# Kernel tuning notes

Measured on AMD Instinct MI355X. Metric: run time of the kernel, lower is better.

## Reference

```python
import jax, jax.numpy as jnp
import numpy as np
import math

N = 8192        # n_cells
D_IN = 512      # input_dim
D_H = 1024      # hidden_dim
N_F = 8         # min(8, N//2)
FS = N // N_F   # faction size
SYNC = 0.15
DEBATE = 0.15
TWO_PI = 2.0 * math.pi


def setup_inputs() -> dict:
    key = jax.random.key(0)
    ks = jax.random.split(key, 10)
    phases = jax.random.uniform(ks[0], (N,), dtype=jnp.float32) * TWO_PI
    omegas = jax.random.normal(ks[1], (N,), dtype=jnp.float32) * 0.5 + 1.0
    coupling = jax.random.normal(ks[2], (N, N), dtype=jnp.float32) * 0.01
    K = jnp.asarray(2.0, dtype=jnp.float32)
    # Linear weights stored as [in, out]
    w_p2h = jax.random.normal(ks[3], (2, D_H), dtype=jnp.float32) * (1.0 / math.sqrt(2.0))
    b_p2h = jnp.zeros((D_H,), dtype=jnp.float32)
    w_enc1 = jax.random.normal(ks[4], (D_H + D_IN, D_H), dtype=jnp.float32) * (1.0 / math.sqrt(D_H + D_IN))
    b_enc1 = jnp.zeros((D_H,), dtype=jnp.float32)
    w_enc2 = jax.random.normal(ks[5], (D_H, D_H), dtype=jnp.float32) * (1.0 / math.sqrt(D_H))
    b_enc2 = jnp.zeros((D_H,), dtype=jnp.float32)
    w_out = jax.random.normal(ks[6], (D_H, D_IN), dtype=jnp.float32) * (1.0 / math.sqrt(D_H))
    b_out = jnp.zeros((D_IN,), dtype=jnp.float32)
    x = jax.random.normal(ks[7], (D_IN,), dtype=jnp.float32)
    return {"x": x, "phases": phases, "omegas": omegas, "coupling": coupling, "K": K,
            "w_p2h": w_p2h, "b_p2h": b_p2h, "w_enc1": w_enc1, "b_enc1": b_enc1,
            "w_enc2": w_enc2, "b_enc2": b_enc2, "w_out": w_out, "b_out": b_out,
            "step": 10}


def _forward(x, phases, omegas, coupling, K, w_p2h, b_p2h, w_enc1, b_enc1,
             w_enc2, b_enc2, w_out, b_out, step):
    # --- kuramoto_step (torch runs it under no_grad) ---
    input_mag = jax.lax.stop_gradient(jnp.linalg.norm(x))
    phase_diff = phases[:, None] - phases[None, :]                 # [N, N]
    coupling_eff = jax.nn.sigmoid(coupling) * K / N                # [N, N]
    interactions = (coupling_eff * jnp.sin(phase_diff)).sum(axis=1)
    dtheta = omegas + interactions + input_mag * 0.1
    phases_new = jax.lax.stop_gradient((phases + 0.1 * dtheta) % TWO_PI)
    sin_p, cos_p = jnp.sin(phases_new), jnp.cos(phases_new)
    r = jnp.sqrt(cos_p.mean() ** 2 + sin_p.mean() ** 2)
    tension = jnp.abs(r - 0.5) * 2.0                               # scalar (non-diff, .item() in torch)

    # --- phase features -> per-cell hidden ---
    phase_features = jnp.stack([sin_p, cos_p], axis=-1)            # [N, 2]
    cell_hiddens = phase_features @ w_p2h + b_p2h                  # [N, D_H]

    # --- faction_sync_debate, vectorized over the 8 factions ---
    h = cell_hiddens.reshape(N_F, FS, D_H)
    fmean = h.mean(axis=1, keepdims=True)                          # [N_F, 1, D_H]
    h = (1.0 - SYNC) * h + SYNC * fmean
    if step > 5:  # step is a static Python int
        global_opinion = h.mean(axis=1).mean(axis=0)               # [D_H]
        dc = max(1, FS // 4)
        h = h.at[:, :dc].set((1.0 - DEBATE) * h[:, :dc] + DEBATE * global_opinion)
    cell_hiddens = h.reshape(N, D_H)

    # --- encode with broadcast input ---
    x_b = jnp.broadcast_to(x, (N, D_IN))
    combined = jnp.concatenate([cell_hiddens, x_b], axis=-1)       # [N, D_H + D_IN]
    encoded = jnp.tanh(combined @ w_enc1 + b_enc1) @ w_enc2 + b_enc2

    # --- coherence-weighted readout ---
    mean_phase = jnp.arctan2(sin_p.mean(), cos_p.mean())
    coherence = jnp.cos(phases_new - mean_phase)                   # [N]
    weights = jax.nn.softmax(coherence * 5.0)
    weighted = (weights[:, None] * encoded).sum(axis=0, keepdims=True)  # [1, D_H]
    output = weighted @ w_out + b_out                              # [1, D_IN]
    return output, tension


def reference(x, phases, omegas, coupling, K, w_p2h, b_p2h, w_enc1, b_enc1,
              w_enc2, b_enc2, w_out, b_out, step):
    return _forward(x, phases, omegas, coupling, K, w_p2h, b_p2h, w_enc1,
                    b_enc1, w_enc2, b_enc2, w_out, b_out, step)
```

## Files before the change

kernel.cpp:

```cpp
#include <hip/hip_runtime.h>
#include <math.h>


#define NC   8192
#define DH   1024
#define DIN  512

using f4 = __attribute__((ext_vector_type(4))) float;

constexpr int IMG = 0, TENS = 6, CNT = 7;
constexpr int SN0 = 32;
constexpr int CN0 = SN0 + NC;
constexpr int SNN = CN0 + NC;
constexpr int CNN = SNN + NC;
constexpr int UPART  = CNN + NC;
constexpr int UFIN   = UPART + 16 * 3 * DH;
constexpr int TPART  = UFIN + 3 * DH;
constexpr int W2PART = TPART + 128 * DH;
constexpr int OPART  = W2PART + 16 * DH;

__device__ __forceinline__ float frcp(float x) { return __builtin_amdgcn_rcpf(x); }
__device__ __forceinline__ float sigm(float x) { return frcp(1.f + __expf(-x)); }
__device__ __forceinline__ float ftanh(float x) { return 1.f - 2.f * frcp(__expf(2.f * x) + 1.f); }

template <int BS>
__device__ __forceinline__ float block_reduce(float v, float* sh) {
  #pragma unroll
  for (int m = 1; m < 64; m <<= 1) v += __shfl_xor(v, m, 64);
  constexpr int NW = BS / 64;
  int lane = threadIdx.x & 63, w = threadIdx.x >> 6;
  if (lane == 0) sh[w] = v;
  __syncthreads();
  if (w == 0) {
    float x = (lane < NW) ? sh[lane] : 0.f;
    #pragma unroll
    for (int m = 1; m < NW; m <<= 1) x += __shfl_xor(x, m, 64);
    if (lane == 0) sh[0] = x;
  }
  __syncthreads();
  float r = sh[0];
  __syncthreads();
  return r;
}

__global__ __launch_bounds__(256) void k_prep_up(const float* __restrict__ phases,
                                                 const float* __restrict__ x,
                                                 const float* __restrict__ w_p2h,
                                                 const float* __restrict__ b_p2h,
                                                 const float* __restrict__ w_enc1,
                                                 const float* __restrict__ b_enc1,
                                                 float* __restrict__ W) {
  __shared__ float sh[4];
  int b = blockIdx.x, t = threadIdx.x;
  if (b < 32) {
    int i = b * 256 + t;
    float s, c;
    sincosf(phases[i], &s, &c);
    W[SN0 + i] = s;
    W[CN0 + i] = c;
  } else if (b == 32) {
    float x0 = x[t], x1 = x[t + 256];
    float v = block_reduce<256>(x0 * x0 + x1 * x1, sh);
    if (t == 0) W[IMG] = sqrtf(v);
  } else {
    int dy = b - 33;
    f4 a0 = {0.f, 0.f, 0.f, 0.f}, a1 = a0, a2 = a0;
    for (int d = dy * 64; d < dy * 64 + 64; ++d) {
      f4 r = *(const f4*)(w_enc1 + (size_t)d * DH + 4 * t);
      float s0 = w_p2h[d], s1 = w_p2h[DH + d], s2 = b_p2h[d];
      #pragma unroll
      for (int e = 0; e < 4; ++e) {
        a0[e] = fmaf(s0, r[e], a0[e]);
        a1[e] = fmaf(s1, r[e], a1[e]);
        a2[e] = fmaf(s2, r[e], a2[e]);
      }
    }
    for (int k = dy * 32; k < dy * 32 + 32; ++k) {
      f4 r = *(const f4*)(w_enc1 + (size_t)(DH + k) * DH + 4 * t);
      float xv = x[k];
      #pragma unroll
      for (int e = 0; e < 4; ++e) a2[e] = fmaf(xv, r[e], a2[e]);
    }
    if (dy == 0) {
      f4 bb = *(const f4*)(b_enc1 + 4 * t);
      #pragma unroll
      for (int e = 0; e < 4; ++e) a2[e] += bb[e];
    }
    float* up = W + UPART + dy * 3 * DH;
    *(f4*)(up + 4 * t) = a0;
    *(f4*)(up + DH + 4 * t) = a1;
    *(f4*)(up + 2 * DH + 4 * t) = a2;
  }
}

__global__ __launch_bounds__(256) void k_rows(const float* __restrict__ coupling,
                                              const float* __restrict__ phases,
                                              const float* __restrict__ omegas,
                                              const float* __restrict__ Kp,
                                              float* __restrict__ W) {
  __shared__ float sh[4][4];
  int t = threadIdx.x;
  int row0 = blockIdx.x * 2;
  const f4* c0 = (const f4*)(coupling + (size_t)row0 * NC);
  const f4* c1 = (const f4*)(coupling + (size_t)(row0 + 1) * NC);
  const f4* s4 = (const f4*)(W + SN0);
  const f4* c4 = (const f4*)(W + CN0);
  float sc0 = 0.f, ss0 = 0.f, sc1 = 0.f, ss1 = 0.f;
  #pragma unroll 4
  for (int k = 0; k < 8; ++k) {
    int idx = k * 256 + t;
    f4 cc = c4[idx];
    f4 sv = s4[idx];
    f4 v0 = __builtin_nontemporal_load(c0 + idx);
    f4 v1 = __builtin_nontemporal_load(c1 + idx);
    #pragma unroll
    for (int e = 0; e < 4; ++e) {
      float g0 = sigm(v0[e]);
      sc0 = fmaf(g0, cc[e], sc0);
      ss0 = fmaf(g0, sv[e], ss0);
      float g1 = sigm(v1[e]);
      sc1 = fmaf(g1, cc[e], sc1);
      ss1 = fmaf(g1, sv[e], ss1);
    }
  }
  #pragma unroll
  for (int m = 1; m < 64; m <<= 1) {
    sc0 += __shfl_xor(sc0, m, 64);
    ss0 += __shfl_xor(ss0, m, 64);
    sc1 += __shfl_xor(sc1, m, 64);
    ss1 += __shfl_xor(ss1, m, 64);
  }
  int lane = t & 63, w = t >> 6;
  if (lane == 0) { sh[w][0] = sc0; sh[w][1] = ss0; sh[w][2] = sc1; sh[w][3] = ss1; }
  __syncthreads();
  if (t < 2) {
    float sc = sh[0][2 * t] + sh[1][2 * t] + sh[2][2 * t] + sh[3][2 * t];
    float ss = sh[0][2 * t + 1] + sh[1][2 * t + 1] + sh[2][2 * t + 1] + sh[3][2 * t + 1];
    int row = row0 + t;
    float kk = Kp[0];
    float si = W[SN0 + row], ci = W[CN0 + row];
    float inter = (kk / (float)NC) * (si * sc - ci * ss);
    float dtheta = omegas[row] + inter + 0.1f * W[IMG];
    float pn = phases[row] + 0.1f * dtheta;
    float s, c;
    sincosf(pn, &s, &c);
    W[SNN + row] = s;
    W[CNN + row] = c;
  }
}

__global__ __launch_bounds__(1024) void k_stats_ured(float* __restrict__ W) {
  if (blockIdx.x > 0) {
    int j = (blockIdx.x - 1) * 1024 + threadIdx.x;
    float v = 0.f;
    #pragma unroll
    for (int p = 0; p < 16; ++p) v += W[UPART + p * 3 * DH + j];
    W[UFIN + j] = v;
    return;
  }
  __shared__ float shS[16], shC[16], shD[16], shMP[2];
  int t = threadIdx.x, lane = t & 63, w = t >> 6;
  int f = w >> 1, half = w & 1;
  int base = f * 1024 + half * 512;
  float s = 0.f, c = 0.f;
  #pragma unroll
  for (int k = 0; k < 8; ++k) {
    int i = base + k * 64 + lane;
    s += W[SNN + i];
    c += W[CNN + i];
  }
  #pragma unroll
  for (int m = 1; m < 64; m <<= 1) {
    s += __shfl_xor(s, m, 64);
    c += __shfl_xor(c, m, 64);
  }
  if (lane == 0) { shS[w] = s; shC[w] = c; }
  __syncthreads();
  if (t == 0) {
    float ssum = 0.f, csum = 0.f;
    #pragma unroll
    for (int ff = 0; ff < 8; ++ff) {
      float S = shS[2 * ff] + shS[2 * ff + 1];
      float C = shC[2 * ff] + shC[2 * ff + 1];
      W[8 + ff] = S * (1.f / 1024.f);
      W[16 + ff] = C * (1.f / 1024.f);
      ssum += S;
      csum += C;
    }
    float sbar = ssum * (1.f / (float)NC);
    float cbar = csum * (1.f / (float)NC);
    float mp = atan2f(sbar, cbar);
    float mpc = cosf(mp), mps = sinf(mp);
    W[1] = sbar; W[2] = cbar; W[3] = mpc; W[4] = mps;
    float r = sqrtf(cbar * cbar + sbar * sbar);
    W[TENS] = fabsf(r - 0.5f) * 2.f;
    shMP[0] = mpc; shMP[1] = mps;
  }
  __syncthreads();
  float mpc = shMP[0], mps = shMP[1];
  float d = 0.f;
  #pragma unroll
  for (int k = 0; k < 8; ++k) {
    int i = k * 1024 + t;
    float coh = W[CNN + i] * mpc + W[SNN + i] * mps;
    d += __expf(5.f * coh - 5.f);
  }
  #pragma unroll
  for (int m = 1; m < 64; m <<= 1) d += __shfl_xor(d, m, 64);
  if (lane == 0) shD[w] = d;
  __syncthreads();
  if (t == 0) {
    float D = 0.f;
    #pragma unroll
    for (int ww = 0; ww < 16; ++ww) D += shD[ww];
    W[5] = D;
  }
}

__global__ __launch_bounds__(256) void k_cells(const int* __restrict__ step,
                                               float* __restrict__ W) {
  int t = threadIdx.x, b = blockIdx.x;
  float u0[4], u1[4], u2[4], acc[4] = {0.f, 0.f, 0.f, 0.f};
  #pragma unroll
  for (int k = 0; k < 4; ++k) {
    int h = t + k * 256;
    u0[k] = W[UFIN + h];
    u1[k] = W[UFIN + DH + h];
    u2[k] = W[UFIN + 2 * DH + h];
  }
  bool debate = step[0] > 5;
  float sbar = W[1], cbar = W[2], mpc = W[3], mps = W[4];
  float invden = 1.0f / W[5];
  int i0 = b * 64;
  int f = i0 >> 10;
  float Sf = W[8 + f], Cf = W[16 + f];
  bool deb = debate && ((i0 & 1023) < 256);
  for (int j = 0; j < 64; ++j) {
    int i = i0 + j;
    float s = W[SNN + i], c = W[CNN + i];
    float a = fmaf(0.15f, Sf, 0.85f * s);
    float bb = fmaf(0.15f, Cf, 0.85f * c);
    if (deb) {
      a = fmaf(0.15f, sbar, 0.85f * a);
      bb = fmaf(0.15f, cbar, 0.85f * bb);
    }
    float coh = c * mpc + s * mps;
    float wgt = __expf(5.f * coh - 5.f) * invden;
    #pragma unroll
    for (int k = 0; k < 4; ++k) {
      float pre = fmaf(a, u0[k], fmaf(bb, u1[k], u2[k]));
      acc[k] = fmaf(wgt, ftanh(pre), acc[k]);
    }
  }
  #pragma unroll
  for (int k = 0; k < 4; ++k) W[TPART + b * DH + t + k * 256] = acc[k];
}

__global__ __launch_bounds__(256) void k_wv(const float* __restrict__ w_enc2,
                                            const float* __restrict__ b_enc2,
                                            float* __restrict__ W) {
  __shared__ float ts[64];
  int t = threadIdx.x, cb = blockIdx.x, hb = blockIdx.y;
  if (t == 0 && cb == 0 && hb == 0) *(unsigned*)(W + CNT) = 0u;
  if (t < 64) {
    int h = hb * 64 + t;
    float v = 0.f;
    for (int p = 0; p < 128; ++p) v += W[TPART + p * DH + h];
    ts[t] = v;
  }
  __syncthreads();
  int c = cb * 256 + t;
  float acc = (hb == 0) ? b_enc2[c] : 0.f;
  #pragma unroll 8
  for (int j = 0; j < 64; ++j) acc = fmaf(ts[j], w_enc2[(hb * 64 + j) * DH + c], acc);
  W[W2PART + hb * DH + c] = acc;
}

__global__ __launch_bounds__(256) void k_out(const float* __restrict__ w_out,
                                             const float* __restrict__ b_out,
                                             float* __restrict__ W,
                                             float* __restrict__ out) {
  __shared__ float wv[64];
  __shared__ int last;
  int t = threadIdx.x, ob = blockIdx.x, cb = blockIdx.y;
  if (t < 64) {
    int c = cb * 64 + t;
    float v = 0.f;
    #pragma unroll
    for (int p = 0; p < 16; ++p) v += W[W2PART + p * DH + c];
    wv[t] = v;
  }
  __syncthreads();
  int o = ob * 256 + t;
  float acc = 0.f;
  #pragma unroll 8
  for (int j = 0; j < 64; ++j) acc = fmaf(wv[j], w_out[(cb * 64 + j) * DIN + o], acc);
  W[OPART + cb * DIN + o] = acc;
  __syncthreads();
  if (t == 0) {
    unsigned old = __hip_atomic_fetch_add((unsigned*)(W + CNT), 1u,
                                          __ATOMIC_ACQ_REL, __HIP_MEMORY_SCOPE_AGENT);
    last = (old == 31u);
  }
  __syncthreads();
  if (!last) return;
  for (int oo = t; oo < DIN; oo += 256) {
    float a = b_out[oo];
    #pragma unroll
    for (int p = 0; p < 16; ++p) a += W[OPART + p * DIN + oo];
    out[oo] = a;
  }
  if (t == 0) out[DIN] = W[TENS];
}

extern "C" void kernel_launch(void* const* d_in, const int* in_sizes, int n_in,
                              void* d_out, int out_size, void* d_ws, size_t ws_size,
                              hipStream_t stream) {
  (void)in_sizes; (void)n_in; (void)out_size; (void)ws_size;
  const float* x        = (const float*)d_in[0];
  const float* phases   = (const float*)d_in[1];
  const float* omegas   = (const float*)d_in[2];
  const float* coupling = (const float*)d_in[3];
  const float* Kp       = (const float*)d_in[4];
  const float* w_p2h    = (const float*)d_in[5];
  const float* b_p2h    = (const float*)d_in[6];
  const float* w_enc1   = (const float*)d_in[7];
  const float* b_enc1   = (const float*)d_in[8];
  const float* w_enc2   = (const float*)d_in[9];
  const float* b_enc2   = (const float*)d_in[10];
  const float* w_out    = (const float*)d_in[11];
  const float* b_out    = (const float*)d_in[12];
  const int*   step     = (const int*)d_in[13];
  float* W   = (float*)d_ws;
  float* out = (float*)d_out;

  k_prep_up   <<<49, 256, 0, stream>>>(phases, x, w_p2h, b_p2h, w_enc1, b_enc1, W);
  k_rows      <<<NC / 2, 256, 0, stream>>>(coupling, phases, omegas, Kp, W);
  k_stats_ured<<<4, 1024, 0, stream>>>(W);
  k_cells     <<<128, 256, 0, stream>>>(step, W);
  k_wv        <<<dim3(4, 16), 256, 0, stream>>>(w_enc2, b_enc2, W);
  k_out       <<<dim3(2, 16), 256, 0, stream>>>(w_out, b_out, W, out);
}
```

Before: 91.05 us.

## Fuse prep kernel into row kernel and recompute sin/cos of phases inline

```diff
diff --git a/kernel.cpp b/kernel.cpp
--- a/kernel.cpp
+++ b/kernel.cpp
@@ -8,10 +8,8 @@
 
 using f4 = __attribute__((ext_vector_type(4))) float;
 
-constexpr int IMG = 0, TENS = 6, CNT = 7;
-constexpr int SN0 = 32;
-constexpr int CN0 = SN0 + NC;
-constexpr int SNN = CN0 + NC;
+constexpr int TENS = 6, CNT = 7;
+constexpr int SNN = 32 + 2 * NC;
 constexpr int CNN = SNN + NC;
 constexpr int UPART  = CNN + NC;
 constexpr int UFIN   = UPART + 16 * 3 * DH;
@@ -23,47 +21,19 @@
 __device__ __forceinline__ float sigm(float x) { return frcp(1.f + __expf(-x)); }
 __device__ __forceinline__ float ftanh(float x) { return 1.f - 2.f * frcp(__expf(2.f * x) + 1.f); }
 
-template <int BS>
-__device__ __forceinline__ float block_reduce(float v, float* sh) {
-  #pragma unroll
-  for (int m = 1; m < 64; m <<= 1) v += __shfl_xor(v, m, 64);
-  constexpr int NW = BS / 64;
-  int lane = threadIdx.x & 63, w = threadIdx.x >> 6;
-  if (lane == 0) sh[w] = v;
-  __syncthreads();
-  if (w == 0) {
-    float x = (lane < NW) ? sh[lane] : 0.f;
-    #pragma unroll
-    for (int m = 1; m < NW; m <<= 1) x += __shfl_xor(x, m, 64);
-    if (lane == 0) sh[0] = x;
-  }
-  __syncthreads();
-  float r = sh[0];
-  __syncthreads();
-  return r;
-}
-
-__global__ __launch_bounds__(256) void k_prep_up(const float* __restrict__ phases,
-                                                 const float* __restrict__ x,
-                                                 const float* __restrict__ w_p2h,
-                                                 const float* __restrict__ b_p2h,
-                                                 const float* __restrict__ w_enc1,
-                                                 const float* __restrict__ b_enc1,
-                                                 float* __restrict__ W) {
-  __shared__ float sh[4];
-  int b = blockIdx.x, t = threadIdx.x;
-  if (b < 32) {
-    int i = b * 256 + t;
-    float s, c;
-    sincosf(phases[i], &s, &c);
-    W[SN0 + i] = s;
-    W[CN0 + i] = c;
-  } else if (b == 32) {
-    float x0 = x[t], x1 = x[t + 256];
-    float v = block_reduce<256>(x0 * x0 + x1 * x1, sh);
-    if (t == 0) W[IMG] = sqrtf(v);
-  } else {
-    int dy = b - 33;
+__global__ __launch_bounds__(256) void k_rows_all(const float* __restrict__ coupling,
+                                                  const float* __restrict__ phases,
+                                                  const float* __restrict__ omegas,
+                                                  const float* __restrict__ Kp,
+                                                  const float* __restrict__ x,
+                                                  const float* __restrict__ w_p2h,
+                                                  const float* __restrict__ b_p2h,
+                                                  const float* __restrict__ w_enc1,
+                                                  const float* __restrict__ b_enc1,
+                                                  float* __restrict__ W) {
+  int t = threadIdx.x;
+  if (blockIdx.x >= 4096) {
+    int dy = blockIdx.x - 4096;
     f4 a0 = {0.f, 0.f, 0.f, 0.f}, a1 = a0, a2 = a0;
     for (int d = dy * 64; d < dy * 64 + 64; ++d) {
       f4 r = *(const f4*)(w_enc1 + (size_t)d * DH + 4 * t);
@@ -90,37 +60,41 @@
     *(f4*)(up + 4 * t) = a0;
     *(f4*)(up + DH + 4 * t) = a1;
     *(f4*)(up + 2 * DH + 4 * t) = a2;
-  }
-}
-
-__global__ __launch_bounds__(256) void k_rows(const float* __restrict__ coupling,
-                                              const float* __restrict__ phases,
-                                              const float* __restrict__ omegas,
-                                              const float* __restrict__ Kp,
-                                              float* __restrict__ W) {
+    return;
+  }
+  __shared__ float shn[4];
   __shared__ float sh[4][4];
-  int t = threadIdx.x;
+  int lane = t & 63, w = t >> 6;
+  {
+    float x0 = x[t], x1 = x[t + 256];
+    float v = x0 * x0 + x1 * x1;
+    #pragma unroll
+    for (int m = 1; m < 64; m <<= 1) v += __shfl_xor(v, m, 64);
+    if (lane == 0) shn[w] = v;
+  }
+  __syncthreads();
+  float img = sqrtf((shn[0] + shn[1]) + (shn[2] + shn[3]));
   int row0 = blockIdx.x * 2;
   const f4* c0 = (const f4*)(coupling + (size_t)row0 * NC);
   const f4* c1 = (const f4*)(coupling + (size_t)(row0 + 1) * NC);
-  const f4* s4 = (const f4*)(W + SN0);
-  const f4* c4 = (const f4*)(W + CN0);
+  const f4* p4 = (const f4*)phases;
   float sc0 = 0.f, ss0 = 0.f, sc1 = 0.f, ss1 = 0.f;
-  #pragma unroll 4
+  #pragma unroll 2
   for (int k = 0; k < 8; ++k) {
     int idx = k * 256 + t;
-    f4 cc = c4[idx];
-    f4 sv = s4[idx];
+    f4 ph = p4[idx];
     f4 v0 = __builtin_nontemporal_load(c0 + idx);
     f4 v1 = __builtin_nontemporal_load(c1 + idx);
     #pragma unroll
     for (int e = 0; e < 4; ++e) {
+      float sv, cc;
+      __sincosf(ph[e], &sv, &cc);
       float g0 = sigm(v0[e]);
-      sc0 = fmaf(g0, cc[e], sc0);
-      ss0 = fmaf(g0, sv[e], ss0);
+      sc0 = fmaf(g0, cc, sc0);
+      ss0 = fmaf(g0, sv, ss0);
       float g1 = sigm(v1[e]);
-      sc1 = fmaf(g1, cc[e], sc1);
-      ss1 = fmaf(g1, sv[e], ss1);
+      sc1 = fmaf(g1, cc, sc1);
+      ss1 = fmaf(g1, sv, ss1);
     }
   }
   #pragma unroll
@@ -130,7 +104,6 @@
     sc1 += __shfl_xor(sc1, m, 64);
     ss1 += __shfl_xor(ss1, m, 64);
   }
-  int lane = t & 63, w = t >> 6;
   if (lane == 0) { sh[w][0] = sc0; sh[w][1] = ss0; sh[w][2] = sc1; sh[w][3] = ss1; }
   __syncthreads();
   if (t < 2) {
@@ -138,9 +111,10 @@
     float ss = sh[0][2 * t + 1] + sh[1][2 * t + 1] + sh[2][2 * t + 1] + sh[3][2 * t + 1];
     int row = row0 + t;
     float kk = Kp[0];
-    float si = W[SN0 + row], ci = W[CN0 + row];
+    float si, ci;
+    sincosf(phases[row], &si, &ci);
     float inter = (kk / (float)NC) * (si * sc - ci * ss);
-    float dtheta = omegas[row] + inter + 0.1f * W[IMG];
+    float dtheta = omegas[row] + inter + 0.1f * img;
     float pn = phases[row] + 0.1f * dtheta;
     float s, c;
     sincosf(pn, &s, &c);
@@ -334,8 +308,8 @@
   float* W   = (float*)d_ws;
   float* out = (float*)d_out;
 
-  k_prep_up   <<<49, 256, 0, stream>>>(phases, x, w_p2h, b_p2h, w_enc1, b_enc1, W);
-  k_rows      <<<NC / 2, 256, 0, stream>>>(coupling, phases, omegas, Kp, W);
+  k_rows_all  <<<4112, 256, 0, stream>>>(coupling, phases, omegas, Kp, x,
+                                         w_p2h, b_p2h, w_enc1, b_enc1, W);
   k_stats_ured<<<4, 1024, 0, stream>>>(W);
   k_cells     <<<128, 256, 0, stream>>>(step, W);
   k_wv        <<<dim3(4, 16), 256, 0, stream>>>(w_enc2, b_enc2, W);
```

After: 89.75 us. About the same (-1.4%).
